# Kernel tuning notes

Hardware: AMD Instinct MI355X
Metric: run time of the kernel (lower is better)

Reference implementation:

```python
import jax, jax.numpy as jnp
import numpy as np

BS, NQ, D = 4, 12500, 256
HEADS, LEVELS, POINTS = 8, 2, 4
HD = D // HEADS
D_FF = 2048
SHAPES = ((100, 100), (50, 50))   # (H, W) per level; sum(H*W) == NQ
STARTS = (0, 10000)


def layer_norm(x, g, b, eps=1e-5):
    m = x.mean(-1, keepdims=True)
    v = ((x - m) ** 2).mean(-1, keepdims=True)
    return (x - m) * jax.lax.rsqrt(v + eps) * g + b


def bilinear_sample(value_l, loc, H, W):
    # value_l: (bs, heads, H*W, hd); loc: (bs, heads, nq, P, 2) normalized [0,1]
    # matches F.grid_sample(align_corners=False, padding_mode='zeros')
    x = loc[..., 0] * W - 0.5
    y = loc[..., 1] * H - 0.5
    x0 = jnp.floor(x)
    y0 = jnp.floor(y)
    wx1 = x - x0
    wy1 = y - y0
    wx0 = 1.0 - wx1
    wy0 = 1.0 - wy1
    x0i = x0.astype(jnp.int32)
    y0i = y0.astype(jnp.int32)

    def gather(xi, yi):
        valid = (xi >= 0) & (xi < W) & (yi >= 0) & (yi < H)
        idx = jnp.clip(yi, 0, H - 1) * W + jnp.clip(xi, 0, W - 1)  # (bs,heads,nq,P)
        b, h, nq, P = idx.shape
        g = jnp.take_along_axis(value_l, idx.reshape(b, h, nq * P, 1), axis=2)
        g = g.reshape(b, h, nq, P, -1)
        return g * valid[..., None].astype(g.dtype)

    g00 = gather(x0i, y0i)
    g10 = gather(x0i + 1, y0i)
    g01 = gather(x0i, y0i + 1)
    g11 = gather(x0i + 1, y0i + 1)
    return (g00 * (wx0 * wy0)[..., None] + g10 * (wx1 * wy0)[..., None]
            + g01 * (wx0 * wy1)[..., None] + g11 * (wx1 * wy1)[..., None])


def setup_inputs() -> dict:
    key = jax.random.key(0)
    ks = jax.random.split(key, 20)
    s = 0.02
    inp = {
        'query': jax.random.normal(ks[0], (BS, NQ, D), jnp.float32),
        'reference_points': jax.random.uniform(ks[1], (BS, NQ, LEVELS, 2), jnp.float32),
        'w_off': s * jax.random.normal(ks[2], (D, HEADS * LEVELS * POINTS * 2), jnp.float32),
        'b_off': s * jax.random.normal(ks[3], (HEADS * LEVELS * POINTS * 2,), jnp.float32),
        'w_attn': s * jax.random.normal(ks[4], (D, HEADS * LEVELS * POINTS), jnp.float32),
        'b_attn': s * jax.random.normal(ks[5], (HEADS * LEVELS * POINTS,), jnp.float32),
        'w_val': s * jax.random.normal(ks[6], (D, D), jnp.float32),
        'b_val': jnp.zeros((D,), jnp.float32),
        'w_out': s * jax.random.normal(ks[7], (D, D), jnp.float32),
        'b_out': jnp.zeros((D,), jnp.float32),
        'w1': s * jax.random.normal(ks[8], (D, D_FF), jnp.float32),
        'b1': jnp.zeros((D_FF,), jnp.float32),
        'w2': s * jax.random.normal(ks[9], (D_FF, D), jnp.float32),
        'b2': jnp.zeros((D,), jnp.float32),
        'ln0_g': jnp.ones((D,), jnp.float32),
        'ln0_b': jnp.zeros((D,), jnp.float32),
        'ln1_g': jnp.ones((D,), jnp.float32),
        'ln1_b': jnp.zeros((D,), jnp.float32),
    }
    return inp


def reference(query, reference_points, w_off, b_off, w_attn, b_attn, w_val, b_val,
              w_out, b_out, w1, b1, w2, b2, ln0_g, ln0_b, ln1_g, ln1_b):
    bs, nq, _ = query.shape
    # value projection; encoder self-attention: value == query tokens
    value = (query @ w_val + b_val).reshape(bs, nq, HEADS, HD).transpose(0, 2, 1, 3)  # (bs,heads,nv,hd)
    off = (query @ w_off + b_off).reshape(bs, nq, HEADS, LEVELS, POINTS, 2)
    aw = (query @ w_attn + b_attn).reshape(bs, nq, HEADS, LEVELS * POINTS)
    aw = jax.nn.softmax(aw, axis=-1).reshape(bs, nq, HEADS, LEVELS, POINTS)

    out = jnp.zeros((bs, HEADS, nq, HD), query.dtype)
    for l, (H, W) in enumerate(SHAPES):
        normalizer = jnp.array([W, H], query.dtype)
        # (bs,nq,heads,P,2)
        loc = reference_points[:, :, None, l, None, :] + off[:, :, :, l] / normalizer
        loc = loc.transpose(0, 2, 1, 3, 4)  # (bs,heads,nq,P,2)
        v_l = value[:, :, STARTS[l]:STARTS[l] + H * W]  # (bs,heads,H*W,hd)
        sampled = bilinear_sample(v_l, loc, H, W)       # (bs,heads,nq,P,hd)
        w_l = aw[:, :, :, l].transpose(0, 2, 1, 3)      # (bs,heads,nq,P)
        out = out + (sampled * w_l[..., None]).sum(axis=3)

    attn_out = out.transpose(0, 2, 1, 3).reshape(bs, nq, D) @ w_out + b_out
    x = layer_norm(query + attn_out, ln0_g, ln0_b)
    h = jax.nn.relu(x @ w1 + b1)
    x = layer_norm(x + (h @ w2 + b2), ln1_g, ln1_b)
    return x
```

## Files before the change

kernel.cpp:

```cpp
#include <hip/hip_runtime.h>


#define NQv 12500
#define BSv 4
#define Dv  256
#define DFF 2048

typedef __attribute__((ext_vector_type(8))) __bf16 bf16x8;
typedef __attribute__((ext_vector_type(4))) float f32x4;

__device__ __forceinline__ ushort f32_to_bf16(float f) {
  unsigned u = __float_as_uint(f);
  u += 0x7FFFu + ((u >> 16) & 1u);
  return (ushort)(u >> 16);
}
__device__ __forceinline__ float bf16_to_f32(ushort u) {
  return __uint_as_float(((unsigned)u) << 16);
}

__global__ __launch_bounds__(256) void conv_bf16_kernel(
    const float* __restrict__ in, ushort* __restrict__ out, int n4) {
  int i = blockIdx.x * 256 + threadIdx.x;
  if (i >= n4) return;
  float4 v = reinterpret_cast<const float4*>(in)[i];
  uint2 st;
  st.x = (unsigned)f32_to_bf16(v.x) | ((unsigned)f32_to_bf16(v.y) << 16);
  st.y = (unsigned)f32_to_bf16(v.z) | ((unsigned)f32_to_bf16(v.w) << 16);
  reinterpret_cast<uint2*>(out)[i] = st;
}

__global__ __launch_bounds__(256) void build_wcat_kernel(
    const float* __restrict__ w_val, const float* __restrict__ w_off,
    const float* __restrict__ w_attn, const float* __restrict__ b_val,
    const float* __restrict__ b_off, const float* __restrict__ b_attn,
    ushort* __restrict__ wcat, float* __restrict__ bcat) {
  int i = blockIdx.x * 256 + threadIdx.x;
  if (i < 448 * 256) {
    int n = i >> 8, k = i & 255;
    float v = (n < 256) ? w_val[(size_t)k * 256 + n]
              : (n < 384) ? w_off[(size_t)k * 128 + (n - 256)]
                          : w_attn[(size_t)k * 64 + (n - 384)];
    wcat[i] = f32_to_bf16(v);
  }
  if (i < 512)
    bcat[i] = (i < 256) ? b_val[i] : (i < 384) ? b_off[i - 256]
              : (i < 448) ? b_attn[i - 384] : 0.f;
}

template <int MODE>
__global__ __launch_bounds__(256) void ttrans_stage_kernel(
    const float* __restrict__ src, ushort* __restrict__ dst, int N) {
  __shared__ ushort tl[64][65];
  const int k0 = blockIdx.y * 64, n0 = blockIdx.x * 64;
  const int t = threadIdx.x;
#pragma unroll
  for (int i = 0; i < 16; ++i) {
    int idx = t + 256 * i;
    int kk = idx >> 6, nn = idx & 63;
    tl[kk][nn] = f32_to_bf16(src[(size_t)(k0 + kk) * N + n0 + nn]);
  }
  __syncthreads();
#pragma unroll
  for (int i = 0; i < 16; ++i) {
    int idx = t + 256 * i;
    int off = idx & 511;
    int nn = off >> 3, kl = off & 7;
    if (MODE == 0) {
      int s = idx >> 9;
      int kk = s * 8 + kl;
      int g = (n0 >> 7) * 4 + (k0 >> 6);
      dst[(size_t)g * 8192 + s * 1024 + (n0 & 64) * 8 + off] = tl[kk][nn];
    } else {
      int gl = idx >> 11;
      int s = (idx >> 9) & 3;
      int kk = gl * 32 + s * 8 + kl;
      int g = (MODE == 1) ? ((k0 >> 7) * 4 + ((k0 & 64) >> 5) + gl)
                          : ((k0 >> 5) + gl);
      dst[(size_t)g * 8192 + s * 2048 + (size_t)(n0 + nn) * 8 + kl] = tl[kk][nn];
    }
  }
}

#define TBM 128
#define TBN 128
#define TBK 32

template <int RELU, int NMASK, int SPLIT>
__global__ __launch_bounds__(256) void gemm128_kernel(
    const ushort* __restrict__ A, const ushort* __restrict__ Bt,
    const float* __restrict__ bias, ushort* __restrict__ C,
    ushort* __restrict__ C2,
    int M, int K, int ldc, int Nreal) {
  __shared__ ushort lds[4][TBM * TBK];

  const int t = threadIdx.x;
  const int wid = t >> 6, lane = t & 63;
  const int wr = wid >> 1, wc = wid & 1;

  const int nwg = gridDim.x * gridDim.y;
  const int lbid = blockIdx.y * gridDim.x + blockIdx.x;
  const int q = nwg >> 3, r = nwg & 7;
  const int xcd = lbid & 7, li = lbid >> 3;
  const int wgid = (xcd < r ? xcd * (q + 1) : r * (q + 1) + (xcd - r) * q) + li;
  const int m0 = (wgid / gridDim.x) * TBM;
  const int n0 = (wgid % gridDim.x) * TBN;

  int srowA[2], srowB[2], gsl[2];
#pragma unroll
  for (int i = 0; i < 2; i++) {
    int row = i * 64 + (t >> 2);
    int ar = m0 + row;
    srowA[i] = (ar < M) ? ar : (M - 1);
    srowB[i] = n0 + row;
    gsl[i] = ((t & 3) ^ ((row >> 1) & 3)) * 8;
  }

  f32x4 acc[4][4] = {};
  const int nt = K / TBK;
  int cur = 0;

#pragma unroll
  for (int i = 0; i < 2; i++) {
    const int ldsoff = (i * 256 + wid * 64) * 8;
    __builtin_amdgcn_global_load_lds(
        (const __attribute__((address_space(1))) void*)(A + (size_t)srowA[i] * K + gsl[i]),
        (__attribute__((address_space(3))) void*)(lds[0] + ldsoff), 16, 0, 0);
    __builtin_amdgcn_global_load_lds(
        (const __attribute__((address_space(1))) void*)(Bt + (size_t)srowB[i] * K + gsl[i]),
        (__attribute__((address_space(3))) void*)(lds[1] + ldsoff), 16, 0, 0);
  }
  __syncthreads();

  const int rl = lane & 15, kh = lane >> 4;
  for (int tk = 0; tk < nt; ++tk) {
    if (tk + 1 < nt) {
      const int k0 = (tk + 1) * TBK;
      const int nb = (cur ^ 1) * 2;
#pragma unroll
      for (int i = 0; i < 2; i++) {
        const int ldsoff = (i * 256 + wid * 64) * 8;
        __builtin_amdgcn_global_load_lds(
            (const __attribute__((address_space(1))) void*)(A + (size_t)srowA[i] * K + k0 + gsl[i]),
            (__attribute__((address_space(3))) void*)(lds[nb] + ldsoff), 16, 0, 0);
        __builtin_amdgcn_global_load_lds(
            (const __attribute__((address_space(1))) void*)(Bt + (size_t)srowB[i] * K + k0 + gsl[i]),
            (__attribute__((address_space(3))) void*)(lds[nb + 1] + ldsoff), 16, 0, 0);
      }
    }
    {
      const ushort* As = lds[cur * 2];
      const ushort* Bs = lds[cur * 2 + 1];
      bf16x8 afr[4], bfr[4];
#pragma unroll
      for (int ni = 0; ni < 4; ni++) {
        int rowb = wc * 64 + ni * 16 + rl;
        int p = kh ^ ((rowb >> 1) & 3);
        bfr[ni] = *reinterpret_cast<const bf16x8*>(Bs + rowb * 32 + p * 8);
      }
#pragma unroll
      for (int mi = 0; mi < 4; mi++) {
        int rowa = wr * 64 + mi * 16 + rl;
        int p = kh ^ ((rowa >> 1) & 3);
        afr[mi] = *reinterpret_cast<const bf16x8*>(As + rowa * 32 + p * 8);
      }
#pragma unroll
      for (int mi = 0; mi < 4; mi++)
#pragma unroll
        for (int ni = 0; ni < 4; ni++)
          acc[mi][ni] = __builtin_amdgcn_mfma_f32_16x16x32_bf16(afr[mi], bfr[ni], acc[mi][ni], 0, 0, 0);
    }
    __syncthreads();
    cur ^= 1;
  }

  ushort* ldsC = lds[0];
  const int rgrp = lane >> 4, cl = lane & 15;
#pragma unroll
  for (int pass = 0; pass < 2; ++pass) {
    if (wr == pass) {
#pragma unroll
      for (int mi = 0; mi < 4; mi++) {
#pragma unroll
        for (int ni = 0; ni < 4; ni++) {
          int col = wc * 64 + ni * 16 + cl;
          float bv = bias[n0 + col];
#pragma unroll
          for (int r = 0; r < 4; r++) {
            int rloc = mi * 16 + rgrp * 4 + r;
            float v = acc[mi][ni][r] + bv;
            if (RELU) v = fmaxf(v, 0.f);
            ldsC[rloc * 132 + col] = f32_to_bf16(v);
          }
        }
      }
    }
    __syncthreads();
    {
      int rloc = t >> 2;
      int row = m0 + pass * 64 + rloc;
      if (row < M) {
#pragma unroll
        for (int j = 0; j < 4; j++) {
          int col = (t & 3) * 32 + j * 8;
          uint4 v = *reinterpret_cast<const uint4*>(ldsC + rloc * 132 + col);
          if (SPLIT) {
            int gcol = n0 + col;
            if (gcol < 256)
              *reinterpret_cast<uint4*>(C + (size_t)row * 256 + gcol) = v;
            else if (gcol < 448)
              *reinterpret_cast<uint4*>(C2 + (size_t)row * 192 + (gcol - 256)) = v;
          } else if (!NMASK || n0 + col < Nreal) {
            *reinterpret_cast<uint4*>(C + (size_t)row * ldc + n0 + col) = v;
          }
        }
      }
    }
    __syncthreads();
  }
}

__global__ __launch_bounds__(256, 2) void outproj_ln0_kernel(
    const ushort* __restrict__ samp,
    const ushort* __restrict__ wqf,
    const float* __restrict__ bias,
    const float* __restrict__ query,
    const float* __restrict__ g0, const float* __restrict__ be0,
    ushort* __restrict__ xb,
    int M) {
  __shared__ ushort lds_all[32768];
  ushort* As = lds_all;
  ushort* ring0 = lds_all + 16384;

  const int t = threadIdx.x;
  const int wv = t >> 6;
  const int lane = t & 63;
  const int rl = lane & 15, kq = lane >> 4;
  const int cl = lane & 15, g4 = lane >> 4;
  const int m0 = blockIdx.x * 64;

  ushort* ring[2] = {ring0, ring0 + 8192};

  auto issueB = [&](int j, ushort* dst) {
#pragma unroll
    for (int ii = 0; ii < 4; ++ii) {
      int c = t + 256 * ii;
      __builtin_amdgcn_global_load_lds(
          (const __attribute__((address_space(1))) void*)(wqf + (size_t)j * 8192 + (size_t)c * 8),
          (__attribute__((address_space(3))) void*)(dst + (size_t)c * 8), 16, 0, 0);
    }
  };

#pragma unroll
  for (int ii = 0; ii < 8; ++ii) {
    int c = t + 256 * ii;
    __builtin_amdgcn_global_load_lds(
        (const __attribute__((address_space(1))) void*)(
            samp + (size_t)blockIdx.x * 16384 + (size_t)c * 8),
        (__attribute__((address_space(3))) void*)(As + (size_t)c * 8), 16, 0, 0);
  }
  issueB(0, ring[0]);
  __syncthreads();

  f32x4 accF[4][4] = {};
  int cur = 0;

#pragma unroll
  for (int j = 0; j < 8; ++j) {
    if (j + 1 < 8) issueB(j + 1, ring[cur ^ 1]);
    const ushort* Bs = ring[cur];
    bf16x8 afr[4], bfr[4];
#pragma unroll
    for (int mi = 0; mi < 4; mi++)
      afr[mi] = *reinterpret_cast<const bf16x8*>(As + (j * 4 + kq) * 512 + (mi * 16 + rl) * 8);
#pragma unroll
    for (int ni = 0; ni < 4; ni++)
      bfr[ni] = *reinterpret_cast<const bf16x8*>(Bs + kq * 2048 + (wv * 64 + ni * 16 + rl) * 8);
    __builtin_amdgcn_s_setprio(1);
#pragma unroll
    for (int mi = 0; mi < 4; mi++)
#pragma unroll
      for (int ni = 0; ni < 4; ni++)
        accF[mi][ni] = __builtin_amdgcn_mfma_f32_16x16x32_bf16(afr[mi], bfr[ni], accF[mi][ni], 0, 0, 0);
    __builtin_amdgcn_s_setprio(0);
    __syncthreads();
    cur ^= 1;
  }

  float* ptab = (float*)ring0;
  float* mtab = (float*)(ring0 + 2048);

  float bc[4], gc[4], bec[4];
#pragma unroll
  for (int ni = 0; ni < 4; ni++) {
    int col = wv * 64 + ni * 16 + cl;
    bc[ni] = bias[col]; gc[ni] = g0[col]; bec[ni] = be0[col];
  }
#pragma unroll
  for (int mi = 0; mi < 4; mi++) {
#pragma unroll
    for (int ni = 0; ni < 4; ni++) {
      int col = wv * 64 + ni * 16 + cl;
#pragma unroll
      for (int r = 0; r < 4; r++) {
        int row = mi * 16 + g4 * 4 + r;
        int qrow = m0 + row; qrow = (qrow < M) ? qrow : (M - 1);
        accF[mi][ni][r] += bc[ni] + query[(size_t)qrow * 256 + col];
      }
    }
  }
#pragma unroll
  for (int mi = 0; mi < 4; mi++) {
#pragma unroll
    for (int r = 0; r < 4; r++) {
      float s = accF[mi][0][r] + accF[mi][1][r] + accF[mi][2][r] + accF[mi][3][r];
      float sq = accF[mi][0][r] * accF[mi][0][r] + accF[mi][1][r] * accF[mi][1][r] +
                 accF[mi][2][r] * accF[mi][2][r] + accF[mi][3][r] * accF[mi][3][r];
#pragma unroll
      for (int o = 1; o < 16; o <<= 1) {
        s += __shfl_xor(s, o, 64);
        sq += __shfl_xor(sq, o, 64);
      }
      if (cl == 0) {
        int row = mi * 16 + g4 * 4 + r;
        ptab[(row * 4 + wv) * 2 + 0] = s;
        ptab[(row * 4 + wv) * 2 + 1] = sq;
      }
    }
  }
  __syncthreads();
  {
    int row = t >> 2, part = t & 3;
    float s = ptab[(row * 4 + part) * 2 + 0];
    float sq = ptab[(row * 4 + part) * 2 + 1];
    s += __shfl_xor(s, 1, 64);  sq += __shfl_xor(sq, 1, 64);
    s += __shfl_xor(s, 2, 64);  sq += __shfl_xor(sq, 2, 64);
    if (part == 0) {
      float mean = s * (1.f / 256.f);
      float var = sq * (1.f / 256.f) - mean * mean;
      mtab[row * 2 + 0] = mean;
      mtab[row * 2 + 1] = rsqrtf(var + 1e-5f);
    }
  }
  __syncthreads();
#pragma unroll
  for (int mi = 0; mi < 4; mi++) {
#pragma unroll
    for (int r = 0; r < 4; r++) {
      int row = mi * 16 + g4 * 4 + r;
      float2 ms = *reinterpret_cast<const float2*>(mtab + row * 2);
#pragma unroll
      for (int ni = 0; ni < 4; ni++) {
        int col = wv * 64 + ni * 16 + cl;
        As[(col >> 3) * 512 + row * 8 + (col & 7)] =
            f32_to_bf16((accF[mi][ni][r] - ms.x) * ms.y * gc[ni] + bec[ni]);
      }
    }
  }
  __syncthreads();
  {
    const size_t base128 = (size_t)(blockIdx.x >> 1) * 32768 + (size_t)(blockIdx.x & 1) * 512;
#pragma unroll
    for (int ii = 0; ii < 8; ++ii) {
      int c = t + 256 * ii;
      int s = c >> 6, rl2 = c & 63;
      if (m0 + rl2 < M)
        *reinterpret_cast<uint4*>(xb + base128 + (size_t)s * 1024 + (size_t)rl2 * 8) =
            *reinterpret_cast<const uint4*>(As + (size_t)c * 8);
    }
  }
}

__global__ __launch_bounds__(512, 1) void ffn_ln_fused_kernel(
    const ushort* __restrict__ xb, const ushort* __restrict__ w1f,
    const float* __restrict__ b1, const ushort* __restrict__ w2f,
    const float* __restrict__ b2, const float* __restrict__ g1,
    const float* __restrict__ be1, float* __restrict__ out, int M) {
  __shared__ ushort lds_all[73856];
  ushort* As = lds_all;
  ushort* Hs = lds_all + 32768;
  ushort* stg0 = lds_all + 49280;

  const int t = threadIdx.x;
  const int wv = t >> 6;
  const int wm = wv >> 2;
  const int wn = wv & 3;
  const int lane = t & 63;
  const int rl = lane & 15, kq = lane >> 4;
  const int cl = lane & 15, g4 = lane >> 4;
  const int m0 = blockIdx.x * 128;

  auto stg = [&](int i) { return stg0 + i * 8192; };

  auto issueB1 = [&](int p, int j, ushort* dst) {
    const ushort* src = w1f + (size_t)(p * 4 + j) * 8192;
#pragma unroll
    for (int ii = 0; ii < 2; ++ii) {
      int c = t + 512 * ii;
      __builtin_amdgcn_global_load_lds(
          (const __attribute__((address_space(1))) void*)(src + (size_t)c * 8),
          (__attribute__((address_space(3))) void*)(dst + (size_t)c * 8), 16, 0, 0);
    }
  };
  auto issueB2 = [&](int p, int tt, ushort* dst) {
    const ushort* src = w2f + (size_t)(p * 4 + tt) * 8192;
#pragma unroll
    for (int ii = 0; ii < 2; ++ii) {
      int c = t + 512 * ii;
      __builtin_amdgcn_global_load_lds(
          (const __attribute__((address_space(1))) void*)(src + (size_t)c * 8),
          (__attribute__((address_space(3))) void*)(dst + (size_t)c * 8), 16, 0, 0);
    }
  };

#pragma unroll
  for (int ii = 0; ii < 8; ++ii) {
    int c = t + 512 * ii;
    __builtin_amdgcn_global_load_lds(
        (const __attribute__((address_space(1))) void*)(
            xb + (size_t)blockIdx.x * 32768 + (size_t)c * 8),
        (__attribute__((address_space(3))) void*)(As + (size_t)c * 8), 16, 0, 0);
  }
  issueB1(0, 0, stg(0));
  issueB1(0, 1, stg(1));
  asm volatile("s_waitcnt vmcnt(2)" ::: "memory");
  __builtin_amdgcn_s_barrier();

  f32x4 acc1[4][2] = {};
  f32x4 accF[4][4] = {};
  int cur = 0;

  for (int p = 0; p < 16; ++p) {
#pragma unroll
    for (int j = 0; j < 8; ++j) {
      int tgt = cur + 2; if (tgt >= 3) tgt -= 3;
      if (j <= 5) {
        const int j2 = j + 2;
        const int p2 = p + (j2 >> 3);
        if ((j2 & 7) < 4) issueB1(p2, j2 & 3, stg(tgt));
        else issueB2(p2, (j2 & 7) - 4, stg(tgt));
        asm volatile("s_waitcnt vmcnt(4) lgkmcnt(0)" ::: "memory");
      } else if (p < 15) {
        const int j2m = (j + 2) & 7;
        issueB1(p + 1, j2m, stg(tgt));
        asm volatile("s_waitcnt vmcnt(4) lgkmcnt(0)" ::: "memory");
      } else if (j == 6) {
        asm volatile("s_waitcnt vmcnt(2) lgkmcnt(0)" ::: "memory");
      } else {
        asm volatile("s_waitcnt vmcnt(0) lgkmcnt(0)" ::: "memory");
      }
      __builtin_amdgcn_s_barrier();
      __builtin_amdgcn_sched_barrier(0);

      const ushort* Bs = stg(cur);
      if (j < 4) {
        __builtin_amdgcn_s_setprio(1);
#pragma unroll
        for (int kk = 0; kk < 2; ++kk) {
          bf16x8 afr[4], bfr[2];
          const int slotA = j * 8 + kk * 4 + kq;
#pragma unroll
          for (int mi = 0; mi < 4; mi++)
            afr[mi] = *reinterpret_cast<const bf16x8*>(
                As + slotA * 1024 + (wm * 64 + mi * 16 + rl) * 8);
          const int slotB = kk * 4 + kq;
#pragma unroll
          for (int ni = 0; ni < 2; ni++)
            bfr[ni] = *reinterpret_cast<const bf16x8*>(
                Bs + slotB * 1024 + (wn * 32 + ni * 16 + rl) * 8);
#pragma unroll
          for (int mi = 0; mi < 4; mi++)
#pragma unroll
            for (int ni = 0; ni < 2; ni++)
              acc1[mi][ni] = __builtin_amdgcn_mfma_f32_16x16x32_bf16(afr[mi], bfr[ni], acc1[mi][ni], 0, 0, 0);
        }
        __builtin_amdgcn_s_setprio(0);
        if (j == 3) {
#pragma unroll
          for (int ni = 0; ni < 2; ni++) {
            int col = wn * 32 + ni * 16 + cl;
            float b1v = b1[p * 128 + col];
            const int s = col >> 3, w8 = col & 7;
#pragma unroll
            for (int mi = 0; mi < 4; mi++) {
#pragma unroll
              for (int r = 0; r < 4; r++) {
                int row = wm * 64 + mi * 16 + g4 * 4 + r;
                Hs[s * 1032 + row * 8 + w8] = f32_to_bf16(fmaxf(acc1[mi][ni][r] + b1v, 0.f));
              }
            }
          }
#pragma unroll
          for (int mi = 0; mi < 4; mi++)
#pragma unroll
            for (int ni = 0; ni < 2; ni++)
              acc1[mi][ni] = (f32x4){0.f, 0.f, 0.f, 0.f};
        }
      } else {
        const int tt = j - 4;
        bf16x8 a2f[4], b2f[4];
#pragma unroll
        for (int mi = 0; mi < 4; mi++)
          a2f[mi] = *reinterpret_cast<const bf16x8*>(
              Hs + (tt * 4 + kq) * 1032 + (wm * 64 + mi * 16 + rl) * 8);
#pragma unroll
        for (int ni = 0; ni < 4; ni++)
          b2f[ni] = *reinterpret_cast<const bf16x8*>(
              Bs + kq * 2048 + (wn * 64 + ni * 16 + rl) * 8);
        __builtin_amdgcn_s_setprio(1);
#pragma unroll
        for (int mi = 0; mi < 4; mi++)
#pragma unroll
          for (int ni = 0; ni < 4; ni++)
            accF[mi][ni] = __builtin_amdgcn_mfma_f32_16x16x32_bf16(a2f[mi], b2f[ni], accF[mi][ni], 0, 0, 0);
        __builtin_amdgcn_s_setprio(0);
      }
      cur = cur + 1; if (cur >= 3) cur -= 3;
    }
  }

  float* ptab = (float*)stg0;
  float* mtab = (float*)(stg0 + 2048);

  float b2c[4], g1c[4], bec[4];
#pragma unroll
  for (int ni = 0; ni < 4; ni++) {
    int col = wn * 64 + ni * 16 + cl;
    b2c[ni] = b2[col]; g1c[ni] = g1[col]; bec[ni] = be1[col];
  }
#pragma unroll
  for (int mi = 0; mi < 4; mi++) {
#pragma unroll
    for (int ni = 0; ni < 4; ni++) {
      int col = wn * 64 + ni * 16 + cl;
#pragma unroll
      for (int r = 0; r < 4; r++) {
        int row = wm * 64 + mi * 16 + g4 * 4 + r;
        ushort xv = As[(col >> 3) * 1024 + row * 8 + (col & 7)];
        accF[mi][ni][r] += b2c[ni] + bf16_to_f32(xv);
      }
    }
  }
#pragma unroll
  for (int mi = 0; mi < 4; mi++) {
#pragma unroll
    for (int r = 0; r < 4; r++) {
      float s = accF[mi][0][r] + accF[mi][1][r] + accF[mi][2][r] + accF[mi][3][r];
      float sq = accF[mi][0][r] * accF[mi][0][r] + accF[mi][1][r] * accF[mi][1][r] +
                 accF[mi][2][r] * accF[mi][2][r] + accF[mi][3][r] * accF[mi][3][r];
#pragma unroll
      for (int o = 1; o < 16; o <<= 1) {
        s += __shfl_xor(s, o, 64);
        sq += __shfl_xor(sq, o, 64);
      }
      if (cl == 0) {
        int row = wm * 64 + mi * 16 + g4 * 4 + r;
        ptab[(row * 4 + wn) * 2 + 0] = s;
        ptab[(row * 4 + wn) * 2 + 1] = sq;
      }
    }
  }
  __syncthreads();
  {
    int row = t >> 2, part = t & 3;
    float s = ptab[(row * 4 + part) * 2 + 0];
    float sq = ptab[(row * 4 + part) * 2 + 1];
    s += __shfl_xor(s, 1, 64);  sq += __shfl_xor(sq, 1, 64);
    s += __shfl_xor(s, 2, 64);  sq += __shfl_xor(sq, 2, 64);
    if (part == 0) {
      float mean = s * (1.f / 256.f);
      float var = sq * (1.f / 256.f) - mean * mean;
      mtab[row * 2 + 0] = mean;
      mtab[row * 2 + 1] = rsqrtf(var + 1e-5f);
    }
  }
  __syncthreads();
#pragma unroll
  for (int mi = 0; mi < 4; mi++) {
#pragma unroll
    for (int r = 0; r < 4; r++) {
      int row = wm * 64 + mi * 16 + g4 * 4 + r;
      float2 ms = *reinterpret_cast<const float2*>(mtab + row * 2);
      int grow = m0 + row;
      if (grow < M) {
#pragma unroll
        for (int ni = 0; ni < 4; ni++) {
          int col = wn * 64 + ni * 16 + cl;
          out[(size_t)grow * 256 + col] = (accF[mi][ni][r] - ms.x) * ms.y * g1c[ni] + bec[ni];
        }
      }
    }
  }
}

__global__ __launch_bounds__(256) void deform_attn_kernel(
    const ushort* __restrict__ val,
    const ushort* __restrict__ oa,
    const float* __restrict__ refp,
    ushort* __restrict__ out,
    int R) {
  __shared__ ushort repack[2048];

  const int t = threadIdx.x;
  const int c = t & 3;
  const int h = (t >> 2) & 7;
  const int rloc = t >> 5;
  const int row0 = blockIdx.x * 8;
  const int row = row0 + rloc;

  if (row < R) {
    const int bl = row / NQv;
    const ushort* orow = oa + (size_t)row * 192;

    uint lraw = *reinterpret_cast<const uint*>(orow + 128 + h * 8 + c * 2);
    float l0 = bf16_to_f32((ushort)(lraw & 0xffffu));
    float l1 = bf16_to_f32((ushort)(lraw >> 16));
    float mx = fmaxf(l0, l1);
    mx = fmaxf(mx, __shfl_xor(mx, 1, 64));
    mx = fmaxf(mx, __shfl_xor(mx, 2, 64));
    float e0 = __expf(l0 - mx), e1 = __expf(l1 - mx);
    float sm = e0 + e1;
    sm += __shfl_xor(sm, 1, 64);
    sm += __shfl_xor(sm, 2, 64);
    float inv = 1.f / sm;

    ushort o4[4];
    *reinterpret_cast<uint2*>(o4) = *reinterpret_cast<const uint2*>(orow + h * 16 + c * 4);
    float4 rp = *reinterpret_cast<const float4*>(refp + (size_t)row * 4);
    float Wl = (c & 2) ? 50.f : 100.f;
    float fx = ((c & 2) ? rp.z : rp.x) * Wl - 0.5f;
    float fy = ((c & 2) ? rp.w : rp.y) * Wl - 0.5f;
    float myx0 = fx + bf16_to_f32(o4[0]);
    float myy0 = fy + bf16_to_f32(o4[1]);
    float myx1 = fx + bf16_to_f32(o4[2]);
    float myy1 = fy + bf16_to_f32(o4[3]);
    float myw0 = e0 * inv, myw1 = e1 * inv;

    const int lanebase = (t & 63) & ~3;
    float acc8[8] = {};
#pragma unroll
    for (int p = 0; p < 8; ++p) {
      const int src = lanebase | (p >> 1);
      float x = __shfl((p & 1) ? myx1 : myx0, src, 64);
      float y = __shfl((p & 1) ? myy1 : myy0, src, 64);
      float w = __shfl((p & 1) ? myw1 : myw0, src, 64);
      const int W = (p < 4) ? 100 : 50, H = W;
      const ushort* vbase = val + ((size_t)bl * NQv + ((p < 4) ? 0 : 10000)) * 256 + h * 32 + c * 8;
      float x0f = floorf(x), y0f = floorf(y);
      float wx1 = x - x0f, wy1 = y - y0f;
      float wx0 = 1.f - wx1, wy0 = 1.f - wy1;
      int x0 = (int)x0f, y0 = (int)y0f;
      float cw[4] = {w * wx0 * wy0, w * wx1 * wy0, w * wx0 * wy1, w * wx1 * wy1};
      int cx[4] = {x0, x0 + 1, x0, x0 + 1};
      int cy[4] = {y0, y0, y0 + 1, y0 + 1};
#pragma unroll
      for (int cc = 0; cc < 4; cc++) {
        int xi = cx[cc], yi = cy[cc];
        if (xi >= 0 && xi < W && yi >= 0 && yi < H) {
          ushort vr[8];
          *reinterpret_cast<uint4*>(vr) =
              *reinterpret_cast<const uint4*>(vbase + (size_t)(yi * W + xi) * 256);
          float ww = cw[cc];
#pragma unroll
          for (int j = 0; j < 8; j++) acc8[j] += ww * bf16_to_f32(vr[j]);
        }
      }
    }

    ushort st[8];
#pragma unroll
    for (int j = 0; j < 8; j++) st[j] = f32_to_bf16(acc8[j]);
    *reinterpret_cast<uint4*>(repack + (size_t)(h * 4 + c) * 64 + (size_t)rloc * 8) =
        *reinterpret_cast<uint4*>(st);
  }
  __syncthreads();

  {
    int s2 = t >> 3, r2 = t & 7;
    int grow = row0 + r2;
    if (grow < R) {
      int b64 = row0 >> 6, inner = (row0 & 63) + r2;
      *reinterpret_cast<uint4*>(out + (size_t)b64 * 16384 + (size_t)s2 * 512 + (size_t)inner * 8) =
          *reinterpret_cast<const uint4*>(repack + (size_t)s2 * 64 + (size_t)r2 * 8);
    }
  }
}

extern "C" void kernel_launch(void* const* d_in, const int* in_sizes, int n_in,
                              void* d_out, int out_size, void* d_ws, size_t ws_size,
                              hipStream_t stream) {
  const float* query  = (const float*)d_in[0];
  const float* refp   = (const float*)d_in[1];
  const float* w_off  = (const float*)d_in[2];
  const float* b_off  = (const float*)d_in[3];
  const float* w_attn = (const float*)d_in[4];
  const float* b_attn = (const float*)d_in[5];
  const float* w_val  = (const float*)d_in[6];
  const float* b_val  = (const float*)d_in[7];
  const float* w_out  = (const float*)d_in[8];
  const float* b_out  = (const float*)d_in[9];
  const float* w1     = (const float*)d_in[10];
  const float* b1     = (const float*)d_in[11];
  const float* w2     = (const float*)d_in[12];
  const float* b2     = (const float*)d_in[13];
  const float* ln0g   = (const float*)d_in[14];
  const float* ln0b   = (const float*)d_in[15];
  const float* ln1g   = (const float*)d_in[16];
  const float* ln1b   = (const float*)d_in[17];
  float* outp = (float*)d_out;

  char* ws = (char*)d_ws;
  size_t woff = 0;
  auto walloc = [&](size_t bytes) { size_t r = woff; woff += (bytes + 255) & ~(size_t)255; return r; };
  ushort* wcat = (ushort*)(ws + walloc((size_t)512 * 256 * 2));
  float*  bcat = (float*)(ws + walloc(512 * 4));
  ushort* wqf  = (ushort*)(ws + walloc((size_t)8 * 8192 * 2));
  ushort* w1f  = (ushort*)(ws + walloc((size_t)64 * 8192 * 2));
  ushort* w2f  = (ushort*)(ws + walloc((size_t)64 * 8192 * 2));
  char* arena = ws + woff;
  size_t arena_sz = (ws_size > woff) ? (ws_size - woff) : 0;

  int nb = ((size_t)BSv * NQv * 1920 + (4u << 20) <= arena_sz) ? BSv : 1;
  const int R = nb * NQv;
  const size_t xbsz = (size_t)((R + 127) / 128) * 65536;
  ushort* qb   = (ushort*)arena;
  ushort* valb = (ushort*)(arena + xbsz);
  ushort* oab  = (ushort*)(arena + xbsz + (size_t)R * 512);
  ushort* samp = (ushort*)(arena + xbsz + (size_t)R * 512 + (size_t)R * 384);
  ushort* xb   = qb;

  build_wcat_kernel<<<dim3(448), dim3(256), 0, stream>>>(
      w_val, w_off, w_attn, b_val, b_off, b_attn, wcat, bcat);
  ttrans_stage_kernel<2><<<dim3(4, 4), dim3(256), 0, stream>>>(w_out, wqf, 256);
  ttrans_stage_kernel<0><<<dim3(32, 4), dim3(256), 0, stream>>>(w1, w1f, 2048);
  ttrans_stage_kernel<1><<<dim3(4, 32), dim3(256), 0, stream>>>(w2, w2f, 256);

  const int MT = (R + TBM - 1) / TBM;

  for (int c = 0; c < BSv / nb; c++) {
    const int row0 = c * R;
    const float* qrow = query + (size_t)row0 * Dv;

    conv_bf16_kernel<<<dim3((R * 64 + 255) / 256), dim3(256), 0, stream>>>(qrow, qb, R * 64);

    gemm128_kernel<0, 1, 1><<<dim3(4, MT), dim3(256), 0, stream>>>(
        qb, wcat, bcat, valb, oab, R, Dv, 448, 448);

    deform_attn_kernel<<<dim3((R + 7) / 8), dim3(256), 0, stream>>>(
        valb, oab, refp + (size_t)row0 * 4, samp, R);

    outproj_ln0_kernel<<<dim3((R + 63) / 64), dim3(256), 0, stream>>>(
        samp, wqf, b_out, qrow, ln0g, ln0b, xb, R);

    ffn_ln_fused_kernel<<<dim3((R + 127) / 128), dim3(512), 0, stream>>>(
        xb, w1f, b1, w2f, b2, ln1g, ln1b, outp + (size_t)row0 * 256, R);
  }
}
```

Before: 317.9 us.

## Fuse output projection and LayerNorm0 into the FFN kernel prologue

Merges the out-projection GEMM plus residual/LayerNorm0 kernel into the FFN+LayerNorm1 kernel. Each 512-thread block now computes a 128-row out-projection tile and writes the normalized bf16 result straight into LDS as the FFN A operand. This removes the xb round trip through global memory and one kernel launch. In exchange, the out-projection runs at occupancy 1 with the FFN's large LDS footprint, and the workspace layout is rearranged to match.

```diff
diff --git a/kernel.cpp b/kernel.cpp
--- a/kernel.cpp
+++ b/kernel.cpp
@@ -219,162 +219,18 @@
   }
 }
 
-__global__ __launch_bounds__(256, 2) void outproj_ln0_kernel(
+__global__ __launch_bounds__(512, 1) void attnout_ffn_kernel(
     const ushort* __restrict__ samp,
     const ushort* __restrict__ wqf,
-    const float* __restrict__ bias,
+    const float* __restrict__ b_out,
     const float* __restrict__ query,
     const float* __restrict__ g0, const float* __restrict__ be0,
-    ushort* __restrict__ xb,
-    int M) {
-  __shared__ ushort lds_all[32768];
-  ushort* As = lds_all;
-  ushort* ring0 = lds_all + 16384;
-
-  const int t = threadIdx.x;
-  const int wv = t >> 6;
-  const int lane = t & 63;
-  const int rl = lane & 15, kq = lane >> 4;
-  const int cl = lane & 15, g4 = lane >> 4;
-  const int m0 = blockIdx.x * 64;
-
-  ushort* ring[2] = {ring0, ring0 + 8192};
-
-  auto issueB = [&](int j, ushort* dst) {
-#pragma unroll
-    for (int ii = 0; ii < 4; ++ii) {
-      int c = t + 256 * ii;
-      __builtin_amdgcn_global_load_lds(
-          (const __attribute__((address_space(1))) void*)(wqf + (size_t)j * 8192 + (size_t)c * 8),
-          (__attribute__((address_space(3))) void*)(dst + (size_t)c * 8), 16, 0, 0);
-    }
-  };
-
-#pragma unroll
-  for (int ii = 0; ii < 8; ++ii) {
-    int c = t + 256 * ii;
-    __builtin_amdgcn_global_load_lds(
-        (const __attribute__((address_space(1))) void*)(
-            samp + (size_t)blockIdx.x * 16384 + (size_t)c * 8),
-        (__attribute__((address_space(3))) void*)(As + (size_t)c * 8), 16, 0, 0);
-  }
-  issueB(0, ring[0]);
-  __syncthreads();
-
-  f32x4 accF[4][4] = {};
-  int cur = 0;
-
-#pragma unroll
-  for (int j = 0; j < 8; ++j) {
-    if (j + 1 < 8) issueB(j + 1, ring[cur ^ 1]);
-    const ushort* Bs = ring[cur];
-    bf16x8 afr[4], bfr[4];
-#pragma unroll
-    for (int mi = 0; mi < 4; mi++)
-      afr[mi] = *reinterpret_cast<const bf16x8*>(As + (j * 4 + kq) * 512 + (mi * 16 + rl) * 8);
-#pragma unroll
-    for (int ni = 0; ni < 4; ni++)
-      bfr[ni] = *reinterpret_cast<const bf16x8*>(Bs + kq * 2048 + (wv * 64 + ni * 16 + rl) * 8);
-    __builtin_amdgcn_s_setprio(1);
-#pragma unroll
-    for (int mi = 0; mi < 4; mi++)
-#pragma unroll
-      for (int ni = 0; ni < 4; ni++)
-        accF[mi][ni] = __builtin_amdgcn_mfma_f32_16x16x32_bf16(afr[mi], bfr[ni], accF[mi][ni], 0, 0, 0);
-    __builtin_amdgcn_s_setprio(0);
-    __syncthreads();
-    cur ^= 1;
-  }
-
-  float* ptab = (float*)ring0;
-  float* mtab = (float*)(ring0 + 2048);
-
-  float bc[4], gc[4], bec[4];
-#pragma unroll
-  for (int ni = 0; ni < 4; ni++) {
-    int col = wv * 64 + ni * 16 + cl;
-    bc[ni] = bias[col]; gc[ni] = g0[col]; bec[ni] = be0[col];
-  }
-#pragma unroll
-  for (int mi = 0; mi < 4; mi++) {
-#pragma unroll
-    for (int ni = 0; ni < 4; ni++) {
-      int col = wv * 64 + ni * 16 + cl;
-#pragma unroll
-      for (int r = 0; r < 4; r++) {
-        int row = mi * 16 + g4 * 4 + r;
-        int qrow = m0 + row; qrow = (qrow < M) ? qrow : (M - 1);
-        accF[mi][ni][r] += bc[ni] + query[(size_t)qrow * 256 + col];
-      }
-    }
-  }
-#pragma unroll
-  for (int mi = 0; mi < 4; mi++) {
-#pragma unroll
-    for (int r = 0; r < 4; r++) {
-      float s = accF[mi][0][r] + accF[mi][1][r] + accF[mi][2][r] + accF[mi][3][r];
-      float sq = accF[mi][0][r] * accF[mi][0][r] + accF[mi][1][r] * accF[mi][1][r] +
-                 accF[mi][2][r] * accF[mi][2][r] + accF[mi][3][r] * accF[mi][3][r];
-#pragma unroll
-      for (int o = 1; o < 16; o <<= 1) {
-        s += __shfl_xor(s, o, 64);
-        sq += __shfl_xor(sq, o, 64);
-      }
-      if (cl == 0) {
-        int row = mi * 16 + g4 * 4 + r;
-        ptab[(row * 4 + wv) * 2 + 0] = s;
-        ptab[(row * 4 + wv) * 2 + 1] = sq;
-      }
-    }
-  }
-  __syncthreads();
-  {
-    int row = t >> 2, part = t & 3;
-    float s = ptab[(row * 4 + part) * 2 + 0];
-    float sq = ptab[(row * 4 + part) * 2 + 1];
-    s += __shfl_xor(s, 1, 64);  sq += __shfl_xor(sq, 1, 64);
-    s += __shfl_xor(s, 2, 64);  sq += __shfl_xor(sq, 2, 64);
-    if (part == 0) {
-      float mean = s * (1.f / 256.f);
-      float var = sq * (1.f / 256.f) - mean * mean;
-      mtab[row * 2 + 0] = mean;
-      mtab[row * 2 + 1] = rsqrtf(var + 1e-5f);
-    }
-  }
-  __syncthreads();
-#pragma unroll
-  for (int mi = 0; mi < 4; mi++) {
-#pragma unroll
-    for (int r = 0; r < 4; r++) {
-      int row = mi * 16 + g4 * 4 + r;
-      float2 ms = *reinterpret_cast<const float2*>(mtab + row * 2);
-#pragma unroll
-      for (int ni = 0; ni < 4; ni++) {
-        int col = wv * 64 + ni * 16 + cl;
-        As[(col >> 3) * 512 + row * 8 + (col & 7)] =
-            f32_to_bf16((accF[mi][ni][r] - ms.x) * ms.y * gc[ni] + bec[ni]);
-      }
-    }
-  }
-  __syncthreads();
-  {
-    const size_t base128 = (size_t)(blockIdx.x >> 1) * 32768 + (size_t)(blockIdx.x & 1) * 512;
-#pragma unroll
-    for (int ii = 0; ii < 8; ++ii) {
-      int c = t + 256 * ii;
-      int s = c >> 6, rl2 = c & 63;
-      if (m0 + rl2 < M)
-        *reinterpret_cast<uint4*>(xb + base128 + (size_t)s * 1024 + (size_t)rl2 * 8) =
-            *reinterpret_cast<const uint4*>(As + (size_t)c * 8);
-    }
-  }
-}
-
-__global__ __launch_bounds__(512, 1) void ffn_ln_fused_kernel(
-    const ushort* __restrict__ xb, const ushort* __restrict__ w1f,
-    const float* __restrict__ b1, const ushort* __restrict__ w2f,
-    const float* __restrict__ b2, const float* __restrict__ g1,
-    const float* __restrict__ be1, float* __restrict__ out, int M) {
+    const ushort* __restrict__ w1f,
+    const float* __restrict__ b1,
+    const ushort* __restrict__ w2f,
+    const float* __restrict__ b2,
+    const float* __restrict__ g1, const float* __restrict__ be1,
+    float* __restrict__ out, int M) {
   __shared__ ushort lds_all[73856];
   ushort* As = lds_all;
   ushort* Hs = lds_all + 32768;
@@ -391,6 +247,132 @@
 
   auto stg = [&](int i) { return stg0 + i * 8192; };
 
+  f32x4 accF[4][4] = {};
+
+  {
+    auto issueWq = [&](int j, ushort* dst) {
+#pragma unroll
+      for (int ii = 0; ii < 2; ++ii) {
+        int c = t + 512 * ii;
+        __builtin_amdgcn_global_load_lds(
+            (const __attribute__((address_space(1))) void*)(wqf + (size_t)j * 8192 + (size_t)c * 8),
+            (__attribute__((address_space(3))) void*)(dst + (size_t)c * 8), 16, 0, 0);
+      }
+    };
+#pragma unroll
+    for (int ii = 0; ii < 8; ++ii) {
+      int c = t + 512 * ii;
+      __builtin_amdgcn_global_load_lds(
+          (const __attribute__((address_space(1))) void*)(
+              samp + (size_t)blockIdx.x * 32768 + (size_t)c * 8),
+          (__attribute__((address_space(3))) void*)(As + (size_t)c * 8), 16, 0, 0);
+    }
+    issueWq(0, stg(0));
+    __syncthreads();
+
+    int cur = 0;
+#pragma unroll
+    for (int j = 0; j < 8; ++j) {
+      if (j + 1 < 8) issueWq(j + 1, stg(cur ^ 1));
+      const ushort* Bs = stg(cur);
+      bf16x8 afr[4], bfr[4];
+#pragma unroll
+      for (int mi = 0; mi < 4; mi++)
+        afr[mi] = *reinterpret_cast<const bf16x8*>(
+            As + wm * 16384 + (j * 4 + kq) * 512 + (mi * 16 + rl) * 8);
+#pragma unroll
+      for (int ni = 0; ni < 4; ni++)
+        bfr[ni] = *reinterpret_cast<const bf16x8*>(
+            Bs + kq * 2048 + (wn * 64 + ni * 16 + rl) * 8);
+      __builtin_amdgcn_s_setprio(1);
+#pragma unroll
+      for (int mi = 0; mi < 4; mi++)
+#pragma unroll
+        for (int ni = 0; ni < 4; ni++)
+          accF[mi][ni] = __builtin_amdgcn_mfma_f32_16x16x32_bf16(afr[mi], bfr[ni], accF[mi][ni], 0, 0, 0);
+      __builtin_amdgcn_s_setprio(0);
+      __syncthreads();
+      cur ^= 1;
+    }
+
+    float* ptab = (float*)stg(2);
+    float* mtab = (float*)stg(2) + 1024;
+
+    float bc[4], gc[4], bec[4];
+#pragma unroll
+    for (int ni = 0; ni < 4; ni++) {
+      int col = wn * 64 + ni * 16 + cl;
+      bc[ni] = b_out[col]; gc[ni] = g0[col]; bec[ni] = be0[col];
+    }
+#pragma unroll
+    for (int mi = 0; mi < 4; mi++) {
+#pragma unroll
+      for (int ni = 0; ni < 4; ni++) {
+        int col = wn * 64 + ni * 16 + cl;
+#pragma unroll
+        for (int r = 0; r < 4; r++) {
+          int row = wm * 64 + mi * 16 + g4 * 4 + r;
+          int qrow = m0 + row; qrow = (qrow < M) ? qrow : (M - 1);
+          accF[mi][ni][r] += bc[ni] + query[(size_t)qrow * 256 + col];
+        }
+      }
+    }
+#pragma unroll
+    for (int mi = 0; mi < 4; mi++) {
+#pragma unroll
+      for (int r = 0; r < 4; r++) {
+        float s = accF[mi][0][r] + accF[mi][1][r] + accF[mi][2][r] + accF[mi][3][r];
+        float sq = accF[mi][0][r] * accF[mi][0][r] + accF[mi][1][r] * accF[mi][1][r] +
+                   accF[mi][2][r] * accF[mi][2][r] + accF[mi][3][r] * accF[mi][3][r];
+#pragma unroll
+        for (int o = 1; o < 16; o <<= 1) {
+          s += __shfl_xor(s, o, 64);
+          sq += __shfl_xor(sq, o, 64);
+        }
+        if (cl == 0) {
+          int row = wm * 64 + mi * 16 + g4 * 4 + r;
+          ptab[(row * 4 + wn) * 2 + 0] = s;
+          ptab[(row * 4 + wn) * 2 + 1] = sq;
+        }
+      }
+    }
+    __syncthreads();
+    {
+      int row = t >> 2, part = t & 3;
+      float s = ptab[(row * 4 + part) * 2 + 0];
+      float sq = ptab[(row * 4 + part) * 2 + 1];
+      s += __shfl_xor(s, 1, 64);  sq += __shfl_xor(sq, 1, 64);
+      s += __shfl_xor(s, 2, 64);  sq += __shfl_xor(sq, 2, 64);
+      if (part == 0) {
+        float mean = s * (1.f / 256.f);
+        float var = sq * (1.f / 256.f) - mean * mean;
+        mtab[row * 2 + 0] = mean;
+        mtab[row * 2 + 1] = rsqrtf(var + 1e-5f);
+      }
+    }
+    __syncthreads();
+#pragma unroll
+    for (int mi = 0; mi < 4; mi++) {
+#pragma unroll
+      for (int r = 0; r < 4; r++) {
+        int row = wm * 64 + mi * 16 + g4 * 4 + r;
+        float2 ms = *reinterpret_cast<const float2*>(mtab + row * 2);
+#pragma unroll
+        for (int ni = 0; ni < 4; ni++) {
+          int col = wn * 64 + ni * 16 + cl;
+          As[(col >> 3) * 1024 + row * 8 + (col & 7)] =
+              f32_to_bf16((accF[mi][ni][r] - ms.x) * ms.y * gc[ni] + bec[ni]);
+        }
+      }
+    }
+#pragma unroll
+    for (int mi = 0; mi < 4; mi++)
+#pragma unroll
+      for (int ni = 0; ni < 4; ni++)
+        accF[mi][ni] = (f32x4){0.f, 0.f, 0.f, 0.f};
+    __syncthreads();
+  }
+
   auto issueB1 = [&](int p, int j, ushort* dst) {
     const ushort* src = w1f + (size_t)(p * 4 + j) * 8192;
 #pragma unroll
@@ -412,21 +394,12 @@
     }
   };
 
-#pragma unroll
-  for (int ii = 0; ii < 8; ++ii) {
-    int c = t + 512 * ii;
-    __builtin_amdgcn_global_load_lds(
-        (const __attribute__((address_space(1))) void*)(
-            xb + (size_t)blockIdx.x * 32768 + (size_t)c * 8),
-        (__attribute__((address_space(3))) void*)(As + (size_t)c * 8), 16, 0, 0);
-  }
   issueB1(0, 0, stg(0));
   issueB1(0, 1, stg(1));
   asm volatile("s_waitcnt vmcnt(2)" ::: "memory");
   __builtin_amdgcn_s_barrier();
 
   f32x4 acc1[4][2] = {};
-  f32x4 accF[4][4] = {};
   int cur = 0;
 
   for (int p = 0; p < 16; ++p) {
@@ -721,12 +694,11 @@
 
   int nb = ((size_t)BSv * NQv * 1920 + (4u << 20) <= arena_sz) ? BSv : 1;
   const int R = nb * NQv;
-  const size_t xbsz = (size_t)((R + 127) / 128) * 65536;
+  const size_t smsz = (size_t)((R + 127) / 128) * 65536;
   ushort* qb   = (ushort*)arena;
-  ushort* valb = (ushort*)(arena + xbsz);
-  ushort* oab  = (ushort*)(arena + xbsz + (size_t)R * 512);
-  ushort* samp = (ushort*)(arena + xbsz + (size_t)R * 512 + (size_t)R * 384);
-  ushort* xb   = qb;
+  ushort* valb = (ushort*)(arena + (size_t)R * 512);
+  ushort* oab  = (ushort*)(arena + (size_t)R * 1024);
+  ushort* samp = (ushort*)(arena + (size_t)R * 1408);
 
   build_wcat_kernel<<<dim3(448), dim3(256), 0, stream>>>(
       w_val, w_off, w_attn, b_val, b_off, b_attn, wcat, bcat);
@@ -735,6 +707,7 @@
   ttrans_stage_kernel<1><<<dim3(4, 32), dim3(256), 0, stream>>>(w2, w2f, 256);
 
   const int MT = (R + TBM - 1) / TBM;
+  (void)smsz;
 
   for (int c = 0; c < BSv / nb; c++) {
     const int row0 = c * R;
@@ -748,10 +721,8 @@
     deform_attn_kernel<<<dim3((R + 7) / 8), dim3(256), 0, stream>>>(
         valb, oab, refp + (size_t)row0 * 4, samp, R);
 
-    outproj_ln0_kernel<<<dim3((R + 63) / 64), dim3(256), 0, stream>>>(
-        samp, wqf, b_out, qrow, ln0g, ln0b, xb, R);
-
-    ffn_ln_fused_kernel<<<dim3((R + 127) / 128), dim3(512), 0, stream>>>(
-        xb, w1f, b1, w2f, b2, ln1g, ln1b, outp + (size_t)row0 * 256, R);
-  }
-}
+    attnout_ffn_kernel<<<dim3((R + 127) / 128), dim3(512), 0, stream>>>(
+        samp, wqf, b_out, qrow, ln0g, ln0b, w1f, b1, w2f, b2, ln1g, ln1b,
+        outp + (size_t)row0 * 256, R);
+  }
+}
```

New measurement: 308.6 us. 2.9% less time.
